# Performance work log

Measured on AMD Instinct MI355X. Metric: run time of the kernel, lower is better.

Reference implementation:

```python
import jax, jax.numpy as jnp
import numpy as np
from jax import lax


def _mdlstm_dir(x, Wx, Wh, Wv, b):
    # x: [H, W, B, Cin]; one diagonal-causal 2D-LSTM scan (top-left origin).
    H, W, B, Cin = x.shape
    C = Wh.shape[0]
    xa = jnp.einsum('hwbi,ic->hwbc', x, Wx) + b  # [H,W,B,5C] precomputed input gates

    def col_step(carry, inp):
        h_l, c_l = carry                    # left neighbor [B,C]
        xa_ij, h_u, c_u = inp               # input preact, up neighbor
        a = xa_ij + h_l @ Wh + h_u @ Wv     # [B,5C]
        i, f1, f2, o, g = jnp.split(a, 5, axis=-1)
        c = jax.nn.sigmoid(i) * jnp.tanh(g) + jax.nn.sigmoid(f1) * c_l + jax.nn.sigmoid(f2) * c_u
        h = jax.nn.sigmoid(o) * jnp.tanh(c)
        return (h, c), (h, c)

    z = jnp.zeros((B, C), x.dtype)
    zrow = jnp.zeros((W, B, C), x.dtype)

    def row_step(carry, xa_row):
        h_up, c_up = carry                  # [W,B,C]
        _, (hs, cs) = lax.scan(col_step, (z, z), (xa_row, h_up, c_up))
        return (hs, cs), hs

    _, hh = lax.scan(row_step, (zrow, zrow), xa)  # [H,W,B,C]
    return hh


def _mdlstm4(x, Wx, Wh, Wv, b):
    # x: [B,Cin,H,W] -> per-direction outputs [4,H,W,B,C] (directions: TL, TR, BL, BR origins)
    xt = jnp.transpose(x, (2, 3, 0, 1))  # [H,W,B,Cin]
    x4 = jnp.stack([xt, xt[:, ::-1], xt[::-1], xt[::-1, ::-1]])
    o = jax.vmap(_mdlstm_dir)(x4, Wx, Wh, Wv, b)  # [4,H,W,B,C]
    return jnp.stack([o[0], o[1][:, ::-1], o[2][::-1], o[3][::-1, ::-1]])


def _block(x, Wx, Wh, Wv, b, cw, cb):
    h4 = _mdlstm4(x, Wx, Wh, Wv, b)            # [4,H,W,B,C]
    h = jnp.transpose(h4.sum(0), (2, 3, 0, 1))  # sum directions -> [B,C,H,W]
    y = lax.conv_general_dilated(h, cw, window_strides=(2, 2), padding='VALID',
                                 dimension_numbers=('NCHW', 'OIHW', 'NCHW'))
    return jnp.tanh(y + cb[None, :, None, None])


def _forward(x, p0_Wx, p0_Wh, p0_Wv, p0_b, c0_w, c0_b,
             p1_Wx, p1_Wh, p1_Wv, p1_b, c1_w, c1_b,
             p2_Wx, p2_Wh, p2_Wv, p2_b, dW, db):
    x = _block(x, p0_Wx, p0_Wh, p0_Wv, p0_b, c0_w, c0_b)  # [B,6,31,126]
    x = _block(x, p1_Wx, p1_Wh, p1_Wv, p1_b, c1_w, c1_b)  # [B,20,14,61]
    h4 = _mdlstm4(x, p2_Wx, p2_Wh, p2_Wv, p2_b)           # [4,H,W,B,50]
    # per-direction Linear(50->100) then sum over the 4 directions
    out = jnp.einsum('dhwbc,dcn->bhwn', h4, dW) + db.sum(0)
    return out  # [B,14,61,100]


def setup_inputs() -> dict:
    key = jax.random.key(0)
    ks = jax.random.split(key, 20)
    rn = lambda k, s, sc=0.1: jax.random.normal(k, s, jnp.float32) * sc
    return {
        'x': jax.random.normal(ks[0], (16, 1, 64, 256), jnp.float32),
        'p0_Wx': rn(ks[1], (4, 1, 10)), 'p0_Wh': rn(ks[2], (4, 2, 10)),
        'p0_Wv': rn(ks[3], (4, 2, 10)), 'p0_b': rn(ks[4], (4, 10)),
        'c0_w': rn(ks[5], (6, 2, 2, 4)), 'c0_b': rn(ks[6], (6,)),
        'p1_Wx': rn(ks[7], (4, 6, 50)), 'p1_Wh': rn(ks[8], (4, 10, 50)),
        'p1_Wv': rn(ks[9], (4, 10, 50)), 'p1_b': rn(ks[10], (4, 50)),
        'c1_w': rn(ks[11], (20, 10, 2, 4)), 'c1_b': rn(ks[12], (20,)),
        'p2_Wx': rn(ks[13], (4, 20, 250)), 'p2_Wh': rn(ks[14], (4, 50, 250)),
        'p2_Wv': rn(ks[15], (4, 50, 250)), 'p2_b': rn(ks[16], (4, 250)),
        'dW': rn(ks[17], (4, 50, 100)), 'db': rn(ks[18], (4, 100)),
    }


def reference(x, p0_Wx, p0_Wh, p0_Wv, p0_b, c0_w, c0_b,
              p1_Wx, p1_Wh, p1_Wv, p1_b, c1_w, c1_b,
              p2_Wx, p2_Wh, p2_Wv, p2_b, dW, db):
    return _forward(x, p0_Wx, p0_Wh, p0_Wv, p0_b, c0_w, c0_b,
                    p1_Wx, p1_Wh, p1_Wv, p1_b, c1_w, c1_b,
                    p2_Wx, p2_Wh, p2_Wv, p2_b, dW, db)
```

## Files before the change

### kernel.cpp

```cpp
#include <hip/hip_runtime.h>

typedef unsigned short ushort_t;
typedef __attribute__((ext_vector_type(8))) short short8;
typedef __attribute__((ext_vector_type(4))) float float4_t;
typedef __attribute__((ext_vector_type(2))) float v2f;

__device__ __forceinline__ float frcp(float x) { return __builtin_amdgcn_rcpf(x); }
__device__ __forceinline__ float fsig(float x) { return frcp(1.f + __expf(-x)); }
__device__ __forceinline__ float ftanh(float x) { return 1.f - 2.f * frcp(1.f + __expf(2.f * x)); }
__device__ __forceinline__ float sig_e2(float a) { return frcp(1.f + __builtin_amdgcn_exp2f(a)); }
__device__ __forceinline__ float th_e2(float a) { return 1.f - 2.f * frcp(1.f + __builtin_amdgcn_exp2f(a)); }

__device__ __forceinline__ ushort_t f2bf(float f) {
    union { float f; unsigned u; } v; v.f = f;
    unsigned u = v.u;
    unsigned r = (u + 0x7fffu + ((u >> 16) & 1u)) >> 16;
    return (ushort_t)r;
}
__device__ __forceinline__ float bf2f(ushort_t s) {
    union { unsigned u; float f; } v; v.u = ((unsigned)s) << 16;
    return v.f;
}
__device__ __forceinline__ float dpp_shr1(float x) {
    int i = __builtin_bit_cast(int, x);
    int r = __builtin_amdgcn_update_dpp(0, i, 0x138 , 0xf, 0xf, true);
    return __builtin_bit_cast(float, r);
}

__device__ __forceinline__ void barrier_lds() {
    asm volatile("s_waitcnt lgkmcnt(0)" ::: "memory");
    __builtin_amdgcn_s_barrier();
    asm volatile("" ::: "memory");
}

__global__ __launch_bounds__(128) void k_mdlstm0(
    const float* __restrict__ x, const float* __restrict__ Wx,
    const float* __restrict__ Wh, const float* __restrict__ Wv,
    const float* __restrict__ bias, float* __restrict__ h0)
{
    const int dir = blockIdx.x >> 4, b = blockIdx.x & 15;
    const int tid = threadIdx.x;
    const int u = tid >> 6;
    const int lane = tid & 63;
    const bool fH = dir >= 2, fW = (dir & 1) != 0;
    const int ri = fH ? 63 - lane : lane;
    const float L2E = 1.44269504088896340736f;

    __shared__ float Xs[64 * 256];
    __shared__ float hbuf[2][2][64];
    {
        const float* xg = x + b * 64 * 256;
        for (int i4 = tid; i4 < 4096; i4 += 128) {
            int row = i4 >> 6, c4 = (i4 & 63) << 2;
            float4 v = *(const float4*)(xg + (row << 8) + c4);
            *(float4*)&Xs[(row << 8) + c4] = v;
        }
        for (int i = tid; i < 256; i += 128) ((float*)hbuf)[i] = 0.f;
    }
    __syncthreads();

    float wx[5], bs[5], whS[5], whO[5], wvS[5], wvO[5];
#pragma unroll
    for (int g = 0; g < 5; g++) {
        float sc = (g == 4) ? 2.f * L2E : -L2E;
        int n = g * 2 + u;
        wx[g]  = Wx[dir * 10 + n] * sc;
        bs[g]  = bias[dir * 10 + n] * sc;
        whS[g] = Wh[(dir * 2 + u) * 10 + n] * sc;
        whO[g] = Wh[(dir * 2 + (1 - u)) * 10 + n] * sc;
        wvS[g] = Wv[(dir * 2 + u) * 10 + n] * sc;
        wvO[g] = Wv[(dir * 2 + (1 - u)) * 10 + n] * sc;
    }

    float* orow = h0 + (((dir * 16 + b) * 64 + ri) * 256) * 2 + u;
    float hr = 0.f, cr = 0.f;

    auto ld = [&](int d) -> float {
        int j = d - lane; j = j < 0 ? 0 : (j > 255 ? 255 : j);
        int cj = fW ? 255 - j : j;
        return Xs[(ri << 8) + cj];
    };
    float xp0 = ld(0), xp1 = ld(1);

    int p = 0;
    for (int d = 0; d < 319; d++) {
        float xv = xp0;
        xp0 = xp1;
        xp1 = ld(d + 2);

        float ho  = hbuf[p][1 - u][lane];
        float hus = dpp_shr1(hr);
        float cu  = dpp_shr1(cr);
        float huo = dpp_shr1(ho);

        int j = d - lane;
        if (j >= 0 && j < 256) {
            float a[5];
#pragma unroll
            for (int g = 0; g < 5; g++) {
                float t = fmaf(xv, wx[g], bs[g]);
                t = fmaf(hr,  whS[g], t);
                t = fmaf(ho,  whO[g], t);
                t = fmaf(hus, wvS[g], t);
                t = fmaf(huo, wvO[g], t);
                a[g] = t;
            }
            float si  = sig_e2(a[0]);
            float sf1 = sig_e2(a[1]);
            float sf2 = sig_e2(a[2]);
            float so  = sig_e2(a[3]);
            float tg  = th_e2(a[4]);
            float cn = si * tg + sf1 * cr + sf2 * cu;
            float tc = th_e2(cn * (2.f * L2E));
            hr = so * tc;
            cr = cn;
            int cj = fW ? 255 - j : j;
            orow[cj * 2] = hr;
        } else {
            hr = 0.f;
            cr = 0.f;
        }
        hbuf[1 - p][u][lane] = hr;
        barrier_lds();
        p ^= 1;
    }
}

__global__ __launch_bounds__(128) void k_conv0(
    const float* __restrict__ h0, const float* __restrict__ cw,
    const float* __restrict__ cb, float* __restrict__ x1)
{
    int blk = blockIdx.x;
    int oh = blk / 127, ow = blk % 127;
    int t = threadIdx.x;
    if (t >= 96) return;
    int b = t / 6, co = t % 6;
    float w[2][2][4];
#pragma unroll
    for (int ci = 0; ci < 2; ci++)
#pragma unroll
        for (int kh = 0; kh < 2; kh++)
#pragma unroll
            for (int kw = 0; kw < 4; kw++)
                w[ci][kh][kw] = cw[((co * 2 + ci) * 2 + kh) * 4 + kw];
    float acc = cb[co];
    for (int dirb = 0; dirb < 4; dirb++) {
#pragma unroll
        for (int kh = 0; kh < 2; kh++) {
#pragma unroll
            for (int kw = 0; kw < 4; kw++) {
                const float* ptr = h0 + ((((dirb * 16 + b) * 64) + (2 * oh + kh)) * 256 + (2 * ow + kw)) * 2;
                float2 hv = *(const float2*)ptr;
                acc = fmaf(hv.x, w[0][kh][kw], acc);
                acc = fmaf(hv.y, w[1][kh][kw], acc);
            }
        }
    }
    x1[((oh * 127 + ow) * 16 + b) * 6 + co] = ftanh(acc);
}

__global__ __launch_bounds__(1024, 1) void k_mdlstm1(
    const float* __restrict__ x1, const float* __restrict__ Wx,
    const float* __restrict__ Wh, const float* __restrict__ Wv,
    const float* __restrict__ bias, float* __restrict__ h1)
{
    const int dir = blockIdx.x >> 4, b = blockIdx.x & 15;
    const bool fH = dir >= 2, fW = (dir & 1) != 0;
    const int tid = threadIdx.x;
    const int wave = tid >> 6, lane = tid & 63;

    __shared__ float Xs1[32 * 127 * 6];
    __shared__ __align__(16) ushort_t Ah[2][32][40];
    __shared__ __align__(16) ushort_t Al[2][32][40];
    __shared__ float P[32][68];
    __shared__ float cbuf[2][33][12];

    for (int i = tid; i < 2 * 32 * 40; i += 1024) { ((ushort_t*)Ah)[i] = 0; ((ushort_t*)Al)[i] = 0; }
    for (int i = tid; i < 2 * 33 * 12; i += 1024) ((float*)cbuf)[i] = 0.f;
    for (int i = tid; i < 32 * 127 * 6; i += 1024)
        Xs1[i] = x1[(i / 6) * 96 + b * 6 + (i % 6)];
    __syncthreads();
    if (tid < 6) {
        int rr = fH ? 31 : 0, cc = fW ? 126 : 0;
        float xv = Xs1[(rr * 127 + cc) * 6 + tid];
        ushort_t xh = f2bf(xv);
        Ah[0][0][20 + tid] = xh;
        Al[0][0][20 + tid] = f2bf(xv - bf2f(xh));
    }

    const int mt = wave & 1, nt = wave >> 1;
    short8 bh = {0,0,0,0,0,0,0,0}, bl = {0,0,0,0,0,0,0,0};
    if (wave < 8) {
        int n = nt * 16 + (lane & 15);
#pragma unroll
        for (int jj = 0; jj < 8; jj++) {
            int k = (lane >> 4) * 8 + jj;
            float v = 0.f;
            if (n < 50) {
                if (k < 10)      v = Wh[(dir * 10 + k) * 50 + n];
                else if (k < 20) v = Wv[(dir * 10 + (k - 10)) * 50 + n];
                else if (k < 26) v = Wx[(dir * 6 + (k - 20)) * 50 + n];
            }
            ushort_t hi = f2bf(v);
            bh[jj] = (short)hi;
            bl[jj] = (short)f2bf(v - bf2f(hi));
        }
    }

    const int cell = tid / 10, u = tid % 10;
    float br[5];
#pragma unroll
    for (int g = 0; g < 5; g++) br[g] = (tid < 320) ? bias[dir * 50 + g * 10 + u] : 0.f;
    const int ri = fH ? 31 - cell : cell;
    float creg = 0.f;
    __syncthreads();

    int p = 0;
    for (int d = 0; d < 158; d++) {
        if (wave < 8) {
            const int arow = mt * 16 + (lane & 15);
            const int koff = (lane >> 4) * 8;
            short8 ah = *(const short8*)&Ah[p][arow][koff];
            short8 al = *(const short8*)&Al[p][arow][koff];
            float4_t acc = {0.f, 0.f, 0.f, 0.f};
            acc = __builtin_amdgcn_mfma_f32_16x16x32_bf16(ah, bh, acc, 0, 0, 0);
            acc = __builtin_amdgcn_mfma_f32_16x16x32_bf16(al, bh, acc, 0, 0, 0);
            acc = __builtin_amdgcn_mfma_f32_16x16x32_bf16(ah, bl, acc, 0, 0, 0);
            int col = nt * 16 + (lane & 15);
            int r0 = (lane >> 4) * 4;
#pragma unroll
            for (int r = 0; r < 4; r++) P[mt * 16 + r0 + r][col] = acc[r];
        } else if (tid >= 512 && tid < 704) {
            int s = tid - 512, xc = s / 6, ci = s % 6;
            int jn = d + 1 - xc;
            if (jn >= 0 && jn < 127) {
                int rr = fH ? 31 - xc : xc, cc = fW ? 126 - jn : jn;
                float xv = Xs1[(rr * 127 + cc) * 6 + ci];
                ushort_t xh = f2bf(xv);
                Ah[1 - p][xc][20 + ci] = xh;
                Al[1 - p][xc][20 + ci] = f2bf(xv - bf2f(xh));
            }
        }
        barrier_lds();

        if (tid < 320) {
            int j = d - cell;
            if (j >= 0 && j < 127) {
                float ai  = P[cell][u]      + br[0];
                float af1 = P[cell][10 + u] + br[1];
                float af2 = P[cell][20 + u] + br[2];
                float ao  = P[cell][30 + u] + br[3];
                float ag  = P[cell][40 + u] + br[4];
                float cu = cbuf[p][cell][u];
                float cn = fsig(ai) * ftanh(ag) + fsig(af1) * creg + fsig(af2) * cu;
                float hn = fsig(ao) * ftanh(cn);
                creg = cn;
                cbuf[1 - p][cell + 1][u] = cn;
                ushort_t hh = f2bf(hn);
                float hhf = bf2f(hh);
                ushort_t hlo = f2bf(hn - hhf);
                Ah[1 - p][cell][u] = hh;
                Al[1 - p][cell][u] = hlo;
                if (cell < 31) { Ah[1 - p][cell + 1][10 + u] = hh; Al[1 - p][cell + 1][10 + u] = hlo; }
                int cj = fW ? 126 - j : j;
                h1[(((dir * 16 + b) * 32 + ri) * 127 + cj) * 10 + u] = hn;
            }
        }
        barrier_lds();
        p ^= 1;
    }
}

__global__ __launch_bounds__(320, 1) void k_conv1(
    const float* __restrict__ h1, const float* __restrict__ cw,
    const float* __restrict__ cb, float* __restrict__ x2)
{
    int blk = blockIdx.x;
    int oh = blk / 62, ow = blk % 62;
    int t = threadIdx.x;
    int b = t / 20, co = t % 20;
    float w[10][2][4];
#pragma unroll
    for (int ci = 0; ci < 10; ci++)
#pragma unroll
        for (int kh = 0; kh < 2; kh++)
#pragma unroll
            for (int kw = 0; kw < 4; kw++)
                w[ci][kh][kw] = cw[((co * 10 + ci) * 2 + kh) * 4 + kw];
    float acc = cb[co];
    for (int dirb = 0; dirb < 4; dirb++) {
#pragma unroll
        for (int kh = 0; kh < 2; kh++) {
#pragma unroll
            for (int kw = 0; kw < 4; kw++) {
                const float* ptr = h1 + ((((dirb * 16 + b) * 32) + (2 * oh + kh)) * 127 + (2 * ow + kw)) * 10;
#pragma unroll
                for (int ci = 0; ci < 10; ci++)
                    acc = fmaf(ptr[ci], w[ci][kh][kw], acc);
            }
        }
    }
    x2[((oh * 62 + ow) * 16 + b) * 20 + co] = ftanh(acc);
}

__global__ __launch_bounds__(256) void k_prepB2(
    const float* __restrict__ Wh, const float* __restrict__ Wv,
    const float* __restrict__ Wx, ushort_t* __restrict__ Bh,
    ushort_t* __restrict__ Bl)
{
    int idx = blockIdx.x * 256 + threadIdx.x;
    if (idx >= 131072) return;
    int dir = idx >> 15; int k = (idx >> 8) & 127; int n = idx & 255;
    float v = 0.f;
    if (n < 250) {
        if (k < 50)       v = Wh[(dir * 50 + k) * 250 + n];
        else if (k < 100) v = Wv[(dir * 50 + (k - 50)) * 250 + n];
        else if (k < 120) v = Wx[(dir * 20 + (k - 100)) * 250 + n];
    }
    ushort_t hi = f2bf(v);
    Bh[idx] = hi;
    Bl[idx] = f2bf(v - bf2f(hi));
}

__global__ __launch_bounds__(512, 1) void k_mdlstm2(
    const float* __restrict__ x2, const ushort_t* __restrict__ BmH,
    const ushort_t* __restrict__ BmL,
    const float* __restrict__ bias, float* __restrict__ h2)
{
    const int dir = blockIdx.x >> 4, b = blockIdx.x & 15;
    const bool fH = dir >= 2, fW = (dir & 1) != 0;
    const int tid = threadIdx.x;
    const int wave = tid >> 6, lane = tid & 63;

    __shared__ float Xs2[16 * 62 * 20];
    __shared__ __align__(16) ushort_t Ah[2][16][136];
    __shared__ __align__(16) ushort_t Al[2][16][136];
    __shared__ float P[16][260];
    __shared__ float cbuf[2][16][52];

    for (int i = tid; i < 2 * 16 * 136; i += 512) { ((ushort_t*)Ah)[i] = 0; ((ushort_t*)Al)[i] = 0; }
    for (int i = tid; i < 16 * 62 * 20; i += 512)
        Xs2[i] = x2[(i / 20) * 320 + b * 20 + (i % 20)];
    __syncthreads();
    if (tid < 20) {
        int ci = tid;
        int rr = fH ? 15 : 0, cc = fW ? 61 : 0;
        float xv = Xs2[(rr * 62 + cc) * 20 + ci];
        ushort_t xh = f2bf(xv);
        Ah[0][0][100 + ci] = xh;
        Al[0][0][100 + ci] = f2bf(xv - bf2f(xh));
    }

    short8 bfragH[4][4], bfragL[4][4];
    if (wave < 4) {
#pragma unroll
        for (int j = 0; j < 4; j++) {
            const int n = wave * 64 + j * 16 + (lane & 15);
#pragma unroll
            for (int q = 0; q < 4; q++) {
#pragma unroll
                for (int jj = 0; jj < 8; jj++) {
                    int k = q * 32 + (lane >> 4) * 8 + jj;
                    bfragH[j][q][jj] = (short)BmH[(dir * 128 + k) * 256 + n];
                    bfragL[j][q][jj] = (short)BmL[(dir * 128 + k) * 256 + n];
                }
            }
        }
    }

    const int cell0 = tid / 50, u0 = tid % 50;
    const int cell1 = (512 + tid) / 50, u1 = (512 + tid) % 50;
    float bA0 = bias[dir * 250 + u0];
    float bA1 = bias[dir * 250 + 50 + u0];
    float bA2 = bias[dir * 250 + 100 + u0];
    float bA3 = bias[dir * 250 + 150 + u0];
    float bA4 = bias[dir * 250 + 200 + u0];
    float bB0 = 0, bB1 = 0, bB2 = 0, bB3 = 0, bB4 = 0;
    if (tid < 288) {
        bB0 = bias[dir * 250 + u1];
        bB1 = bias[dir * 250 + 50 + u1];
        bB2 = bias[dir * 250 + 100 + u1];
        bB3 = bias[dir * 250 + 150 + u1];
        bB4 = bias[dir * 250 + 200 + u1];
    }
    const int rrc0 = fH ? 15 - cell0 : cell0;
    const int rrc1 = fH ? 15 - cell1 : cell1;
    float creg0 = 0.f, creg1 = 0.f;
    __syncthreads();

    int p = 0;
    for (int d = 0; d < 77; d++) {
        if (wave < 4) {
            const int arow = lane & 15;
            const int koff = (lane >> 4) * 8;
            short8 ah[4], al[4];
#pragma unroll
            for (int q = 0; q < 4; q++) {
                ah[q] = *(const short8*)&Ah[p][arow][q * 32 + koff];
                al[q] = *(const short8*)&Al[p][arow][q * 32 + koff];
            }
            float4_t acc[4];
#pragma unroll
            for (int j = 0; j < 4; j++) acc[j] = (float4_t){0.f, 0.f, 0.f, 0.f};
#pragma unroll
            for (int q = 0; q < 4; q++)
#pragma unroll
                for (int j = 0; j < 4; j++)
                    acc[j] = __builtin_amdgcn_mfma_f32_16x16x32_bf16(ah[q], bfragH[j][q], acc[j], 0, 0, 0);
#pragma unroll
            for (int q = 0; q < 4; q++)
#pragma unroll
                for (int j = 0; j < 4; j++)
                    acc[j] = __builtin_amdgcn_mfma_f32_16x16x32_bf16(al[q], bfragH[j][q], acc[j], 0, 0, 0);
#pragma unroll
            for (int q = 0; q < 4; q++)
#pragma unroll
                for (int j = 0; j < 4; j++)
                    acc[j] = __builtin_amdgcn_mfma_f32_16x16x32_bf16(ah[q], bfragL[j][q], acc[j], 0, 0, 0);
            const int r0 = (lane >> 4) * 4;
#pragma unroll
            for (int j = 0; j < 4; j++) {
                int col = wave * 64 + j * 16 + (lane & 15);
#pragma unroll
                for (int r = 0; r < 4; r++) P[r0 + r][col] = acc[j][r];
            }
        } else {
            int s = tid - 256;
#pragma unroll
            for (int it = 0; it < 2; it++) {
                int item = s + it * 256;
                if (item < 320) {
                    int xc = item / 20, ci = item % 20;
                    int jn = d + 1 - xc;
                    if (jn >= 0 && jn < 62) {
                        int rr = fH ? 15 - xc : xc, cc = fW ? 61 - jn : jn;
                        float xv = Xs2[(rr * 62 + cc) * 20 + ci];
                        ushort_t xh = f2bf(xv);
                        Ah[1 - p][xc][100 + ci] = xh;
                        Al[1 - p][xc][100 + ci] = f2bf(xv - bf2f(xh));
                    }
                }
            }
        }
        barrier_lds();

        auto gate = [&](int j, int cell, int u, int rrc,
                        float g0, float g1, float g2, float g3, float g4,
                        float& creg) {
            float ai  = P[cell][u] + g0;
            float af1 = P[cell][50 + u] + g1;
            float af2 = P[cell][100 + u] + g2;
            float ao  = P[cell][150 + u] + g3;
            float ag  = P[cell][200 + u] + g4;
            float cu = (cell == 0) ? 0.f : cbuf[p][cell - 1][u];
            float cn = fsig(ai) * ftanh(ag) + fsig(af1) * creg + fsig(af2) * cu;
            float hn = fsig(ao) * ftanh(cn);
            creg = cn;
            cbuf[1 - p][cell][u] = cn;
            ushort_t hh = f2bf(hn);
            float hhf = bf2f(hh);
            ushort_t hlo = f2bf(hn - hhf);
            Ah[1 - p][cell][u] = hh;
            Al[1 - p][cell][u] = hlo;
            if (cell < 15) { Ah[1 - p][cell + 1][50 + u] = hh; Al[1 - p][cell + 1][50 + u] = hlo; }
            int cc = fW ? 61 - j : j;
            h2[(((dir * 16 + b) * 16 + rrc) * 62 + cc) * 50 + u] = hn;
        };
        {
            int j0 = d - cell0;
            if (j0 >= 0 && j0 < 62)
                gate(j0, cell0, u0, rrc0, bA0, bA1, bA2, bA3, bA4, creg0);
            if (tid < 288) {
                int j1 = d - cell1;
                if (j1 >= 0 && j1 < 62)
                    gate(j1, cell1, u1, rrc1, bB0, bB1, bB2, bB3, bB4, creg1);
            }
        }
        barrier_lds();
        p ^= 1;
    }
}

__global__ __launch_bounds__(256) void k_final(
    const float* __restrict__ h2, const float* __restrict__ dW,
    const float* __restrict__ db, float* __restrict__ out)
{
    int blk = blockIdx.x;
    int r = blk / 62, c = blk % 62;
    int t = threadIdx.x;
    __shared__ float hb[3200];
    for (int i = t; i < 3200; i += 256) {
        int dirb = i / 800, rem = i % 800, b = rem / 50, u = rem % 50;
        hb[i] = h2[(((dirb * 16 + b) * 16 + r) * 62 + c) * 50 + u];
    }
    __syncthreads();
    for (int o = t; o < 1600; o += 256) {
        int b = o / 100, n = o % 100;
        float acc = db[n] + db[100 + n] + db[200 + n] + db[300 + n];
#pragma unroll
        for (int dirb = 0; dirb < 4; dirb++) {
            const float* hp = hb + (dirb * 16 + b) * 50;
            const float* wp = dW + dirb * 5000 + n;
#pragma unroll 10
            for (int cc2 = 0; cc2 < 50; cc2++)
                acc = fmaf(hp[cc2], wp[cc2 * 100], acc);
        }
        out[((b * 16 + r) * 62 + c) * 100 + n] = acc;
    }
}

extern "C" void kernel_launch(void* const* d_in, const int* in_sizes, int n_in,
                              void* d_out, int out_size, void* d_ws, size_t ws_size,
                              hipStream_t stream)
{
    const float* x     = (const float*)d_in[0];
    const float* p0_Wx = (const float*)d_in[1];
    const float* p0_Wh = (const float*)d_in[2];
    const float* p0_Wv = (const float*)d_in[3];
    const float* p0_b  = (const float*)d_in[4];
    const float* c0_w  = (const float*)d_in[5];
    const float* c0_b  = (const float*)d_in[6];
    const float* p1_Wx = (const float*)d_in[7];
    const float* p1_Wh = (const float*)d_in[8];
    const float* p1_Wv = (const float*)d_in[9];
    const float* p1_b  = (const float*)d_in[10];
    const float* c1_w  = (const float*)d_in[11];
    const float* c1_b  = (const float*)d_in[12];
    const float* p2_Wx = (const float*)d_in[13];
    const float* p2_Wh = (const float*)d_in[14];
    const float* p2_Wv = (const float*)d_in[15];
    const float* p2_b  = (const float*)d_in[16];
    const float* dW    = (const float*)d_in[17];
    const float* db    = (const float*)d_in[18];
    float* out = (float*)d_out;
    float* ws  = (float*)d_ws;

    float* h0 = ws;
    float* x1 = h0 + 2097152;
    float* h1 = x1 + 390144;
    float* x2 = h1 + 2600960;
    float* h2 = x2 + 317440;
    ushort_t* BmH = (ushort_t*)(h2 + 3174400);
    ushort_t* BmL = BmH + 131072;

    k_prepB2<<<512, 256, 0, stream>>>(p2_Wh, p2_Wv, p2_Wx, BmH, BmL);
    k_mdlstm0<<<64, 128, 0, stream>>>(x, p0_Wx, p0_Wh, p0_Wv, p0_b, h0);
    k_conv0<<<32 * 127, 128, 0, stream>>>(h0, c0_w, c0_b, x1);
    k_mdlstm1<<<64, 1024, 0, stream>>>(x1, p1_Wx, p1_Wh, p1_Wv, p1_b, h1);
    k_conv1<<<16 * 62, 320, 0, stream>>>(h1, c1_w, c1_b, x2);
    k_mdlstm2<<<64, 512, 0, stream>>>(x2, BmH, BmL, p2_b, h2);
    k_final<<<16 * 62, 256, 0, stream>>>(h2, dW, db, out);
}
```

Measured before the change: 474.7 us.

## Replace MFMA split-bf16 gate matmul in layer-1 MDLSTM with per-thread fp32 FMAs

Rewrites the layer-1 MDLSTM wavefront kernel so that each of 320 threads owns one (cell, unit) pair and computes its five gate pre-activations directly with register-resident fp32 weights, using packed v2f FMAs. Weights are pre-scaled by -log2(e) so the activations can use exp2 directly. This removes the MFMA pass, the bf16 hi/lo splitting, the P scratch buffer and one of the two barriers per diagonal step, and shrinks the block from 1024 to 320 threads. In exchange each thread does about 130 scalar FMAs per step and holds many weights in registers.

```diff
diff --git a/kernel.cpp b/kernel.cpp
--- a/kernel.cpp
+++ b/kernel.cpp
@@ -159,7 +159,7 @@
     x1[((oh * 127 + ow) * 16 + b) * 6 + co] = ftanh(acc);
 }
 
-__global__ __launch_bounds__(1024, 1) void k_mdlstm1(
+__global__ __launch_bounds__(320, 1) void k_mdlstm1(
     const float* __restrict__ x1, const float* __restrict__ Wx,
     const float* __restrict__ Wh, const float* __restrict__ Wv,
     const float* __restrict__ bias, float* __restrict__ h1)
@@ -168,104 +168,112 @@
     const bool fH = dir >= 2, fW = (dir & 1) != 0;
     const int tid = threadIdx.x;
     const int wave = tid >> 6, lane = tid & 63;
+    const int u = wave * 2 + (lane >> 5);
+    const int cell = lane & 31;
+    const float L2E = 1.44269504088896340736f;
 
     __shared__ float Xs1[32 * 127 * 6];
-    __shared__ __align__(16) ushort_t Ah[2][32][40];
-    __shared__ __align__(16) ushort_t Al[2][32][40];
-    __shared__ float P[32][68];
-    __shared__ float cbuf[2][33][12];
-
-    for (int i = tid; i < 2 * 32 * 40; i += 1024) { ((ushort_t*)Ah)[i] = 0; ((ushort_t*)Al)[i] = 0; }
-    for (int i = tid; i < 2 * 33 * 12; i += 1024) ((float*)cbuf)[i] = 0.f;
-    for (int i = tid; i < 32 * 127 * 6; i += 1024)
+    __shared__ __align__(16) float hbuf[2][33][14];
+    __shared__ __align__(16) float cbuf[2][33][14];
+
+    for (int i = tid; i < 32 * 127 * 6; i += 320)
         Xs1[i] = x1[(i / 6) * 96 + b * 6 + (i % 6)];
-    __syncthreads();
-    if (tid < 6) {
-        int rr = fH ? 31 : 0, cc = fW ? 126 : 0;
-        float xv = Xs1[(rr * 127 + cc) * 6 + tid];
-        ushort_t xh = f2bf(xv);
-        Ah[0][0][20 + tid] = xh;
-        Al[0][0][20 + tid] = f2bf(xv - bf2f(xh));
-    }
-
-    const int mt = wave & 1, nt = wave >> 1;
-    short8 bh = {0,0,0,0,0,0,0,0}, bl = {0,0,0,0,0,0,0,0};
-    if (wave < 8) {
-        int n = nt * 16 + (lane & 15);
-#pragma unroll
-        for (int jj = 0; jj < 8; jj++) {
-            int k = (lane >> 4) * 8 + jj;
-            float v = 0.f;
-            if (n < 50) {
-                if (k < 10)      v = Wh[(dir * 10 + k) * 50 + n];
-                else if (k < 20) v = Wv[(dir * 10 + (k - 10)) * 50 + n];
-                else if (k < 26) v = Wx[(dir * 6 + (k - 20)) * 50 + n];
-            }
-            ushort_t hi = f2bf(v);
-            bh[jj] = (short)hi;
-            bl[jj] = (short)f2bf(v - bf2f(hi));
-        }
-    }
-
-    const int cell = tid / 10, u = tid % 10;
-    float br[5];
-#pragma unroll
-    for (int g = 0; g < 5; g++) br[g] = (tid < 320) ? bias[dir * 50 + g * 10 + u] : 0.f;
-    const int ri = fH ? 31 - cell : cell;
-    float creg = 0.f;
+    for (int i = tid; i < 2 * 33 * 14; i += 320) {
+        ((float*)hbuf)[i] = 0.f;
+        ((float*)cbuf)[i] = 0.f;
+    }
+
+    v2f wx01[6], wx23[6]; float wx4[6];
+    v2f wh01[10], wh23[10]; float wh4[10];
+    v2f wv01[10], wv23[10]; float wv4[10];
+    v2f bs01, bs23; float bs4;
+    {
+        const float s = -L2E, s4 = 2.f * L2E;
+#pragma unroll
+        for (int c = 0; c < 6; c++) {
+            const float* wp = Wx + (dir * 6 + c) * 50;
+            wx01[c] = (v2f){wp[u] * s, wp[10 + u] * s};
+            wx23[c] = (v2f){wp[20 + u] * s, wp[30 + u] * s};
+            wx4[c]  = wp[40 + u] * s4;
+        }
+#pragma unroll
+        for (int k = 0; k < 10; k++) {
+            const float* wp = Wh + (dir * 10 + k) * 50;
+            wh01[k] = (v2f){wp[u] * s, wp[10 + u] * s};
+            wh23[k] = (v2f){wp[20 + u] * s, wp[30 + u] * s};
+            wh4[k]  = wp[40 + u] * s4;
+            const float* vp = Wv + (dir * 10 + k) * 50;
+            wv01[k] = (v2f){vp[u] * s, vp[10 + u] * s};
+            wv23[k] = (v2f){vp[20 + u] * s, vp[30 + u] * s};
+            wv4[k]  = vp[40 + u] * s4;
+        }
+        const float* bp = bias + dir * 50;
+        bs01 = (v2f){bp[u] * s, bp[10 + u] * s};
+        bs23 = (v2f){bp[20 + u] * s, bp[30 + u] * s};
+        bs4  = bp[40 + u] * s4;
+    }
+
+    const int rr = fH ? 31 - cell : cell;
+    float* orow = h1 + (((dir * 16 + b) * 32 + rr) * 127) * 10 + u;
+    float hr = 0.f, cr = 0.f;
     __syncthreads();
 
     int p = 0;
     for (int d = 0; d < 158; d++) {
-        if (wave < 8) {
-            const int arow = mt * 16 + (lane & 15);
-            const int koff = (lane >> 4) * 8;
-            short8 ah = *(const short8*)&Ah[p][arow][koff];
-            short8 al = *(const short8*)&Al[p][arow][koff];
-            float4_t acc = {0.f, 0.f, 0.f, 0.f};
-            acc = __builtin_amdgcn_mfma_f32_16x16x32_bf16(ah, bh, acc, 0, 0, 0);
-            acc = __builtin_amdgcn_mfma_f32_16x16x32_bf16(al, bh, acc, 0, 0, 0);
-            acc = __builtin_amdgcn_mfma_f32_16x16x32_bf16(ah, bl, acc, 0, 0, 0);
-            int col = nt * 16 + (lane & 15);
-            int r0 = (lane >> 4) * 4;
-#pragma unroll
-            for (int r = 0; r < 4; r++) P[mt * 16 + r0 + r][col] = acc[r];
-        } else if (tid >= 512 && tid < 704) {
-            int s = tid - 512, xc = s / 6, ci = s % 6;
-            int jn = d + 1 - xc;
-            if (jn >= 0 && jn < 127) {
-                int rr = fH ? 31 - xc : xc, cc = fW ? 126 - jn : jn;
-                float xv = Xs1[(rr * 127 + cc) * 6 + ci];
-                ushort_t xh = f2bf(xv);
-                Ah[1 - p][xc][20 + ci] = xh;
-                Al[1 - p][xc][20 + ci] = f2bf(xv - bf2f(xh));
-            }
-        }
-        barrier_lds();
-
-        if (tid < 320) {
-            int j = d - cell;
-            if (j >= 0 && j < 127) {
-                float ai  = P[cell][u]      + br[0];
-                float af1 = P[cell][10 + u] + br[1];
-                float af2 = P[cell][20 + u] + br[2];
-                float ao  = P[cell][30 + u] + br[3];
-                float ag  = P[cell][40 + u] + br[4];
-                float cu = cbuf[p][cell][u];
-                float cn = fsig(ai) * ftanh(ag) + fsig(af1) * creg + fsig(af2) * cu;
-                float hn = fsig(ao) * ftanh(cn);
-                creg = cn;
-                cbuf[1 - p][cell + 1][u] = cn;
-                ushort_t hh = f2bf(hn);
-                float hhf = bf2f(hh);
-                ushort_t hlo = f2bf(hn - hhf);
-                Ah[1 - p][cell][u] = hh;
-                Al[1 - p][cell][u] = hlo;
-                if (cell < 31) { Ah[1 - p][cell + 1][10 + u] = hh; Al[1 - p][cell + 1][10 + u] = hlo; }
-                int cj = fW ? 126 - j : j;
-                h1[(((dir * 16 + b) * 32 + ri) * 127 + cj) * 10 + u] = hn;
-            }
-        }
+        float cu = cbuf[p][cell][u];
+
+        int j = d - cell;
+        if (j >= 0 && j < 127) {
+            int cc = fW ? 126 - j : j;
+            const float* xp = &Xs1[(rr * 127 + cc) * 6];
+            float2 x01 = *(const float2*)(xp);
+            float2 x23 = *(const float2*)(xp + 2);
+            float2 x45 = *(const float2*)(xp + 4);
+            float xv[6] = {x01.x, x01.y, x23.x, x23.y, x45.x, x45.y};
+
+            const float* hlp = &hbuf[p][cell + 1][0];
+            const float* hup = &hbuf[p][cell][0];
+            float hl[10], hu[10];
+#pragma unroll
+            for (int kk = 0; kk < 5; kk++) {
+                float2 t  = *(const float2*)(hlp + 2 * kk);
+                hl[2 * kk] = t.x; hl[2 * kk + 1] = t.y;
+                float2 t2 = *(const float2*)(hup + 2 * kk);
+                hu[2 * kk] = t2.x; hu[2 * kk + 1] = t2.y;
+            }
+
+            v2f a01 = bs01, a23 = bs23; float a4 = bs4;
+#pragma unroll
+            for (int c = 0; c < 6; c++) {
+                v2f xb = {xv[c], xv[c]};
+                a01 = __builtin_elementwise_fma(xb, wx01[c], a01);
+                a23 = __builtin_elementwise_fma(xb, wx23[c], a23);
+                a4  = fmaf(xv[c], wx4[c], a4);
+            }
+#pragma unroll
+            for (int k = 0; k < 10; k++) {
+                v2f hb = {hl[k], hl[k]};
+                a01 = __builtin_elementwise_fma(hb, wh01[k], a01);
+                a23 = __builtin_elementwise_fma(hb, wh23[k], a23);
+                a4  = fmaf(hl[k], wh4[k], a4);
+                v2f ub = {hu[k], hu[k]};
+                a01 = __builtin_elementwise_fma(ub, wv01[k], a01);
+                a23 = __builtin_elementwise_fma(ub, wv23[k], a23);
+                a4  = fmaf(hu[k], wv4[k], a4);
+            }
+            float si  = sig_e2(a01.x), sf1 = sig_e2(a01.y);
+            float sf2 = sig_e2(a23.x), so  = sig_e2(a23.y);
+            float tg  = th_e2(a4);
+            float cn = si * tg + sf1 * cr + sf2 * cu;
+            float tc = th_e2(cn * (2.f * L2E));
+            hr = so * tc;
+            cr = cn;
+            orow[cc * 10] = hr;
+        } else {
+            hr = 0.f; cr = 0.f;
+        }
+        hbuf[1 - p][cell + 1][u] = hr;
+        cbuf[1 - p][cell + 1][u] = cr;
         barrier_lds();
         p ^= 1;
     }
@@ -546,7 +554,7 @@
     k_prepB2<<<512, 256, 0, stream>>>(p2_Wh, p2_Wv, p2_Wx, BmH, BmL);
     k_mdlstm0<<<64, 128, 0, stream>>>(x, p0_Wx, p0_Wh, p0_Wv, p0_b, h0);
     k_conv0<<<32 * 127, 128, 0, stream>>>(h0, c0_w, c0_b, x1);
-    k_mdlstm1<<<64, 1024, 0, stream>>>(x1, p1_Wx, p1_Wh, p1_Wv, p1_b, h1);
+    k_mdlstm1<<<64, 320, 0, stream>>>(x1, p1_Wx, p1_Wh, p1_Wv, p1_b, h1);
     k_conv1<<<16 * 62, 320, 0, stream>>>(h1, c1_w, c1_b, x2);
     k_mdlstm2<<<64, 512, 0, stream>>>(x2, BmH, BmL, p2_b, h2);
     k_final<<<16 * 62, 256, 0, stream>>>(h2, dW, db, out);
```

New measurement: 522.9 us. 1.1x slower.
